# Performance work log

Measured on AMD Instinct MI355X. Metric: run time of the kernel, lower is better.

The kernel has to match this reference:

```python
import jax, jax.numpy as jnp
import numpy as np


def setup_inputs() -> dict:
    key = jax.random.key(0)
    ks = jax.random.split(key, 8)
    C, CK = 512, 64  # channels, att_channels = channels // 8
    B, H, W = 8, 64, 64
    x = jax.random.normal(ks[0], (B, C, H, W), dtype=jnp.float32)
    # 1x1 conv weights stored as [out, in] matrices
    s_in = 1.0 / np.sqrt(C)
    Wf_w = jax.random.uniform(ks[1], (CK, C), jnp.float32, -s_in, s_in)
    Wf_b = jax.random.uniform(ks[2], (CK,), jnp.float32, -s_in, s_in)
    Wg_w = jax.random.uniform(ks[3], (CK, C), jnp.float32, -s_in, s_in)
    Wg_b = jax.random.uniform(ks[4], (CK,), jnp.float32, -s_in, s_in)
    Wh_w = jax.random.uniform(ks[5], (C, C), jnp.float32, -s_in, s_in)
    Wh_b = jax.random.uniform(ks[6], (C,), jnp.float32, -s_in, s_in)
    gamma = jax.random.normal(ks[7], (1,), dtype=jnp.float32) * 0.1
    return {"x": x, "Wf_w": Wf_w, "Wf_b": Wf_b, "Wg_w": Wg_w, "Wg_b": Wg_b,
            "Wh_w": Wh_w, "Wh_b": Wh_b, "gamma": gamma}


def reference(x, Wf_w, Wf_b, Wg_w, Wg_b, Wh_w, Wh_b, gamma):
    B, C, H, W = x.shape
    N = H * W
    xt = x.reshape(B, C, N).transpose(0, 2, 1)           # [B, N, C]
    f = xt @ Wf_w.T + Wf_b                                # [B, N, Ck]
    g = xt @ Wg_w.T + Wg_b                                # [B, N, Ck]
    h = xt @ Wh_w.T + Wh_b                                # [B, N, C]
    scores = jnp.einsum('bnk,bmk->bnm', f, g)             # f @ g^T -> [B, N, N]
    beta = jax.nn.softmax(scores, axis=2)
    o = jnp.einsum('bnm,bmc->bnc', beta, h)               # [B, N, C]
    o = o.transpose(0, 2, 1).reshape(B, C, H, W)
    return gamma[0] * o + x
```

## Files before the change

kernel.cpp:

```cpp
#include <hip/hip_runtime.h>

typedef __attribute__((ext_vector_type(8))) short bf16x8;
typedef __attribute__((ext_vector_type(4))) float f32x4;
typedef __attribute__((ext_vector_type(16))) float f32x16;
typedef unsigned short u16;
typedef unsigned int u32;

namespace {
constexpr int kB = 8;
constexpr int kC = 512;
constexpr int kCK = 64;
constexpr int kN = 4096;

__device__ __forceinline__ u16 f2bf(float f) {
  union { float f; u32 u; } v; v.f = f;
  u32 r = v.u + 0x7fffu + ((v.u >> 16) & 1u);
  return (u16)(r >> 16);
}
__device__ __forceinline__ u32 pk2bf(float a, float b) {
  return (u32)f2bf(a) | ((u32)f2bf(b) << 16);
}
__device__ __forceinline__ f32x4 zero4() { f32x4 z = {0.f, 0.f, 0.f, 0.f}; return z; }
}

__global__ __launch_bounds__(256)
void wcast_kernel(const float* __restrict__ Wf, const float* __restrict__ Wg,
                  const float* __restrict__ Wh, u16* __restrict__ Wcat)
{
  const int idx = blockIdx.x * 256 + threadIdx.x;
  const int e = idx * 4;
  const int row = e >> 9, col = e & 511;
  const float* src = (row < 64) ? &Wf[(size_t)row * 512 + col]
                   : (row < 128) ? &Wg[(size_t)(row - 64) * 512 + col]
                                 : &Wh[(size_t)(row - 128) * 512 + col];
  const float4 v = *(const float4*)src;
  uint2 pk;
  pk.x = pk2bf(v.x, v.y);
  pk.y = pk2bf(v.z, v.w);
  *(uint2*)&Wcat[e] = pk;
}

__global__ __launch_bounds__(256, 2)
void fused_proj_kernel(const float* __restrict__ x, const u16* __restrict__ Wcat,
                       const float* __restrict__ Wf_b, const float* __restrict__ Wg_b,
                       const float* __restrict__ Wh_b,
                       u16* __restrict__ F, u16* __restrict__ G, u16* __restrict__ HT)
{
  const int t = threadIdx.x;
  const int nt = blockIdx.x, b = blockIdx.y;
  const int wave = t >> 6, lane = t & 63, lq = lane & 15, lk = lane >> 4;

  __shared__ __align__(16) u16 xt[64][536];

  const float* xb = x + (size_t)b * kC * kN + (size_t)nt * 64;
  for (int c0 = 0; c0 < kC; c0 += 16) {
    const int c = c0 + wave * 4;
    const size_t base = (size_t)c * kN + lane;
    const float v0 = xb[base];
    const float v1 = xb[base + kN];
    const float v2 = xb[base + 2 * (size_t)kN];
    const float v3 = xb[base + 3 * (size_t)kN];
    uint2 pk; pk.x = pk2bf(v0, v1); pk.y = pk2bf(v2, v3);
    *(uint2*)&xt[lane][c] = pk;
  }
  __syncthreads();

  f32x4 accF[4], accG[4], accH[8][4];
#pragma unroll
  for (int ni = 0; ni < 4; ++ni) { accF[ni] = zero4(); accG[ni] = zero4(); }
#pragma unroll
  for (int cj = 0; cj < 8; ++cj)
#pragma unroll
    for (int ni = 0; ni < 4; ++ni) accH[cj][ni] = zero4();

  for (int ks = 0; ks < 16; ++ks) {
    const int kb = ks * 32 + lk * 8;
    bf16x8 xf[4];
#pragma unroll
    for (int ni = 0; ni < 4; ++ni)
      xf[ni] = *(const bf16x8*)&xt[ni * 16 + lq][kb];

    const bf16x8 wf = *(const bf16x8*)&Wcat[(size_t)(wave * 16 + lq) * 512 + kb];
    const bf16x8 wg = *(const bf16x8*)&Wcat[(size_t)(64 + wave * 16 + lq) * 512 + kb];
    bf16x8 wh[8];
#pragma unroll
    for (int cj = 0; cj < 8; ++cj)
      wh[cj] = *(const bf16x8*)&Wcat[(size_t)(128 + wave * 128 + cj * 16 + lq) * 512 + kb];

#pragma unroll
    for (int ni = 0; ni < 4; ++ni) {
      accF[ni] = __builtin_amdgcn_mfma_f32_16x16x32_bf16(wf, xf[ni], accF[ni], 0, 0, 0);
      accG[ni] = __builtin_amdgcn_mfma_f32_16x16x32_bf16(wg, xf[ni], accG[ni], 0, 0, 0);
#pragma unroll
      for (int cj = 0; cj < 8; ++cj)
        accH[cj][ni] = __builtin_amdgcn_mfma_f32_16x16x32_bf16(xf[ni], wh[cj], accH[cj][ni], 0, 0, 0);
    }
  }

  u16* Fb = F + (size_t)b * kN * kCK;
  u16* Gb = G + (size_t)b * kN * kCK;
  u16* Hb = HT + (size_t)b * kC * kN;

  {
    const float4 bf = *(const float4*)&Wf_b[wave * 16 + lk * 4];
    const float4 bg = *(const float4*)&Wg_b[wave * 16 + lk * 4];
#pragma unroll
    for (int ni = 0; ni < 4; ++ni) {
      const size_t nrow = (size_t)(nt * 64 + ni * 16 + lq);
      uint2 pf, pg;
      pf.x = pk2bf(accF[ni][0] + bf.x, accF[ni][1] + bf.y);
      pf.y = pk2bf(accF[ni][2] + bf.z, accF[ni][3] + bf.w);
      pg.x = pk2bf(accG[ni][0] + bg.x, accG[ni][1] + bg.y);
      pg.y = pk2bf(accG[ni][2] + bg.z, accG[ni][3] + bg.w);
      *(uint2*)&Fb[nrow * kCK + wave * 16 + lk * 4] = pf;
      *(uint2*)&Gb[nrow * kCK + wave * 16 + lk * 4] = pg;
    }
  }
#pragma unroll
  for (int cj = 0; cj < 8; ++cj) {
    const int cout = wave * 128 + cj * 16 + lq;
    const float bh = Wh_b[cout];
#pragma unroll
    for (int ni = 0; ni < 4; ++ni) {
      uint2 ph;
      ph.x = pk2bf(accH[cj][ni][0] + bh, accH[cj][ni][1] + bh);
      ph.y = pk2bf(accH[cj][ni][2] + bh, accH[cj][ni][3] + bh);
      *(uint2*)&Hb[(size_t)cout * kN + nt * 64 + ni * 16 + lk * 4] = ph;
    }
  }
}

__global__ __launch_bounds__(512, 2)
void pv_kernel(const float* __restrict__ x, const u16* __restrict__ F,
               const u16* __restrict__ G, const u16* __restrict__ HT,
               const float* __restrict__ gamma, float* __restrict__ out)
{
  const int t = threadIdx.x;
  const int bid = blockIdx.x;
  const int b  = bid & 7;
  const int qt = bid >> 3;
  const int wave = t >> 6, lane = t & 63;
  const int lq = lane & 15, lk = lane >> 4;
  const int l31 = lane & 31, hi = lane >> 5;

  const int sq2 = wave & 3;
  const int sm2 = wave >> 2;

  const u16* Fb = F + (size_t)b * kN * kCK;
  const u16* Gb = G + (size_t)b * kN * kCK;
  const u16* Hb = HT + (size_t)b * kC * kN;

  __shared__ __align__(16) u16 Ps[2][128][72];
  __shared__ float Lred[2][128];

  const float g0 = gamma[0];

  bf16x8 fF[2][2];
#pragma unroll
  for (int ct = 0; ct < 2; ++ct)
#pragma unroll
    for (int kh = 0; kh < 2; ++kh)
      fF[ct][kh] = *(const bf16x8*)&Fb[(size_t)(qt * 128 + sq2 * 32 + ct * 16 + lq) * kCK + lk * 8 + kh * 32];

  f32x16 acc[2][4];
#pragma unroll
  for (int ci = 0; ci < 2; ++ci)
#pragma unroll
    for (int qb = 0; qb < 4; ++qb)
#pragma unroll
      for (int r = 0; r < 16; ++r) acc[ci][qb][r] = 0.f;

  float lsum[2] = {0.f, 0.f};

  bf16x8 gc[2][2];
#pragma unroll
  for (int ms = 0; ms < 2; ++ms)
#pragma unroll
    for (int kh = 0; kh < 2; ++kh)
      gc[ms][kh] = *(const bf16x8*)&Gb[(size_t)(sm2 * 32 + ms * 16 + lq) * kCK + lk * 8 + kh * 32];

  bf16x8 hc[2][4];

  {
    f32x4 s[2][2];
#pragma unroll
    for (int ms = 0; ms < 2; ++ms)
#pragma unroll
      for (int ct = 0; ct < 2; ++ct) {
        s[ms][ct] = zero4();
        s[ms][ct] = __builtin_amdgcn_mfma_f32_16x16x32_bf16(gc[ms][0], fF[ct][0], s[ms][ct], 0, 0, 0);
        s[ms][ct] = __builtin_amdgcn_mfma_f32_16x16x32_bf16(gc[ms][1], fF[ct][1], s[ms][ct], 0, 0, 0);
      }
#pragma unroll
    for (int ms = 0; ms < 2; ++ms)
#pragma unroll
      for (int kh = 0; kh < 2; ++kh)
        gc[ms][kh] = *(const bf16x8*)&Gb[(size_t)(64 + sm2 * 32 + ms * 16 + lq) * kCK + lk * 8 + kh * 32];
#pragma unroll
    for (int ms = 0; ms < 2; ++ms)
#pragma unroll
      for (int ct = 0; ct < 2; ++ct) {
        const float p0 = __expf(s[ms][ct][0]);
        const float p1 = __expf(s[ms][ct][1]);
        const float p2 = __expf(s[ms][ct][2]);
        const float p3 = __expf(s[ms][ct][3]);
        lsum[ct] += (p0 + p1) + (p2 + p3);
        uint2 pk; pk.x = pk2bf(p0, p1); pk.y = pk2bf(p2, p3);
        *(uint2*)&Ps[0][sq2 * 32 + ct * 16 + lq][sm2 * 32 + ms * 16 + lk * 4] = pk;
      }
#pragma unroll
    for (int ci = 0; ci < 2; ++ci) {
      const size_t hrow = (size_t)(wave * 64 + ci * 32 + l31) * kN;
#pragma unroll
      for (int ks = 0; ks < 4; ++ks)
        hc[ci][ks] = *(const bf16x8*)&Hb[hrow + ks * 16 + hi * 8];
    }
    asm volatile("s_waitcnt lgkmcnt(0)\n\ts_barrier" ::: "memory");
  }

  for (int mt = 1; mt < kN / 64; ++mt) {
    const int pb = (mt - 1) & 1;
    const int buf = mt & 1;

    f32x4 s[2][2];
#pragma unroll
    for (int ms = 0; ms < 2; ++ms)
#pragma unroll
      for (int ct = 0; ct < 2; ++ct) {
        s[ms][ct] = zero4();
        s[ms][ct] = __builtin_amdgcn_mfma_f32_16x16x32_bf16(gc[ms][0], fF[ct][0], s[ms][ct], 0, 0, 0);
        s[ms][ct] = __builtin_amdgcn_mfma_f32_16x16x32_bf16(gc[ms][1], fF[ct][1], s[ms][ct], 0, 0, 0);
      }

    {
      const int mtn = (mt + 1 < kN / 64) ? mt + 1 : mt;
#pragma unroll
      for (int ms = 0; ms < 2; ++ms)
#pragma unroll
        for (int kh = 0; kh < 2; ++kh)
          gc[ms][kh] = *(const bf16x8*)&Gb[(size_t)(mtn * 64 + sm2 * 32 + ms * 16 + lq) * kCK + lk * 8 + kh * 32];
    }

#pragma unroll
    for (int ks = 0; ks < 4; ++ks) {
      bf16x8 pB[4];
#pragma unroll
      for (int qb = 0; qb < 4; ++qb)
        pB[qb] = *(const bf16x8*)&Ps[pb][qb * 32 + l31][ks * 16 + hi * 8];
#pragma unroll
      for (int ci = 0; ci < 2; ++ci)
#pragma unroll
        for (int qb = 0; qb < 4; ++qb)
          acc[ci][qb] = __builtin_amdgcn_mfma_f32_32x32x16_bf16(hc[ci][ks], pB[qb], acc[ci][qb], 0, 0, 0);
      {
        const int ms = ks >> 1, ct = ks & 1;
        const float p0 = __expf(s[ms][ct][0]);
        const float p1 = __expf(s[ms][ct][1]);
        const float p2 = __expf(s[ms][ct][2]);
        const float p3 = __expf(s[ms][ct][3]);
        lsum[ct] += (p0 + p1) + (p2 + p3);
        uint2 pk; pk.x = pk2bf(p0, p1); pk.y = pk2bf(p2, p3);
        *(uint2*)&Ps[buf][sq2 * 32 + ct * 16 + lq][sm2 * 32 + ms * 16 + lk * 4] = pk;
      }
    }

#pragma unroll
    for (int ci = 0; ci < 2; ++ci) {
      const size_t hrow = (size_t)(wave * 64 + ci * 32 + l31) * kN + (size_t)mt * 64;
#pragma unroll
      for (int ks = 0; ks < 4; ++ks)
        hc[ci][ks] = *(const bf16x8*)&Hb[hrow + ks * 16 + hi * 8];
    }

    asm volatile("s_waitcnt lgkmcnt(0)\n\ts_barrier" ::: "memory");
  }

  {
    const int pb = (kN / 64 - 1) & 1;
#pragma unroll
    for (int ks = 0; ks < 4; ++ks) {
      bf16x8 pB[4];
#pragma unroll
      for (int qb = 0; qb < 4; ++qb)
        pB[qb] = *(const bf16x8*)&Ps[pb][qb * 32 + l31][ks * 16 + hi * 8];
#pragma unroll
      for (int ci = 0; ci < 2; ++ci)
#pragma unroll
        for (int qb = 0; qb < 4; ++qb)
          acc[ci][qb] = __builtin_amdgcn_mfma_f32_32x32x16_bf16(hc[ci][ks], pB[qb], acc[ci][qb], 0, 0, 0);
    }
  }

  float l0 = lsum[0], l1 = lsum[1];
  l0 += __shfl_xor(l0, 16); l0 += __shfl_xor(l0, 32);
  l1 += __shfl_xor(l1, 16); l1 += __shfl_xor(l1, 32);
  __syncthreads();
  if (lane < 16) {
    Lred[sm2][sq2 * 32 + lane] = l0;
    Lred[sm2][sq2 * 32 + 16 + lane] = l1;
  }
  __syncthreads();

  float rs[4];
#pragma unroll
  for (int qb = 0; qb < 4; ++qb)
    rs[qb] = 1.f / (Lred[0][qb * 32 + l31] + Lred[1][qb * 32 + l31]);

#pragma unroll
  for (int ci = 0; ci < 2; ++ci)
#pragma unroll
    for (int qb = 0; qb < 4; ++qb)
#pragma unroll
      for (int r = 0; r < 16; ++r) {
        const int crow = (r & 3) + 8 * (r >> 2) + 4 * hi;
        const int c = wave * 64 + ci * 32 + crow;
        const int n = qt * 128 + qb * 32 + l31;
        const size_t idx = ((size_t)b * kC + c) * kN + n;
        out[idx] = g0 * (acc[ci][qb][r] * rs[qb]) + x[idx];
      }
}

extern "C" void kernel_launch(void* const* d_in, const int* in_sizes, int n_in,
                              void* d_out, int out_size, void* d_ws, size_t ws_size,
                              hipStream_t stream)
{
  const float* x     = (const float*)d_in[0];
  const float* Wf_w  = (const float*)d_in[1];
  const float* Wf_b  = (const float*)d_in[2];
  const float* Wg_w  = (const float*)d_in[3];
  const float* Wg_b  = (const float*)d_in[4];
  const float* Wh_w  = (const float*)d_in[5];
  const float* Wh_b  = (const float*)d_in[6];
  const float* gamma = (const float*)d_in[7];
  float* out = (float*)d_out;

  const size_t nF = (size_t)kB * kN * kCK;
  const size_t nH = (size_t)kB * kC * kN;
  const size_t nW = 640 * 512;

  u16* F  = (u16*)d_ws;
  u16* G  = F + nF;
  u16* HT = G + nF;
  u16* Wcat = HT + nH;
  const size_t need = (2 * nF + nH + nW) * sizeof(u16);
  if (ws_size < need) return;

  wcast_kernel<<<dim3(nW / 1024), dim3(256), 0, stream>>>(Wf_w, Wg_w, Wh_w, Wcat);
  fused_proj_kernel<<<dim3(kN / 64, kB), dim3(256), 0, stream>>>(x, Wcat, Wf_b, Wg_b, Wh_b, F, G, HT);
  pv_kernel<<<dim3(256), dim3(512), 0, stream>>>(x, F, G, HT, gamma, out);
}
```

Baseline: 255.5 us.

## Double key tile to 128 and interleave H loads, exp and PV MFMAs

The key-tile width of the fused attention loop grows from 64 to 128, which halves the number of barrier-separated iterations. Score MFMAs are split into two halves per tile, and the H register loads are streamed per k-slice between PV MFMA groups, so global loads, exp/packing and matrix work interleave more finely. s_setprio is raised around the PV MFMA bursts. This enlarges the P shared buffer and adds register pressure, and the hand-ordered schedule may not map onto the hardware as intended.

```diff
diff --git a/kernel.cpp b/kernel.cpp
--- a/kernel.cpp
+++ b/kernel.cpp
@@ -11,6 +11,7 @@
 constexpr int kC = 512;
 constexpr int kCK = 64;
 constexpr int kN = 4096;
+constexpr int kNT = 32;
 
 __device__ __forceinline__ u16 f2bf(float f) {
   union { float f; u32 u; } v; v.f = f;
@@ -150,7 +151,7 @@
   const u16* Gb = G + (size_t)b * kN * kCK;
   const u16* Hb = HT + (size_t)b * kC * kN;
 
-  __shared__ __align__(16) u16 Ps[2][128][72];
+  __shared__ __align__(16) u16 Ps[2][128][136];
   __shared__ float Lred[2][128];
 
   const float g0 = gamma[0];
@@ -173,121 +174,132 @@
   float lsum[2] = {0.f, 0.f};
 
   bf16x8 gc[2][2];
-#pragma unroll
-  for (int ms = 0; ms < 2; ++ms)
-#pragma unroll
-    for (int kh = 0; kh < 2; ++kh)
-      gc[ms][kh] = *(const bf16x8*)&Gb[(size_t)(sm2 * 32 + ms * 16 + lq) * kCK + lk * 8 + kh * 32];
-
   bf16x8 hc[2][4];
+
+#define LOADG(pair, mtile)                                                        \
+  {                                                                               \
+    _Pragma("unroll")                                                             \
+    for (int ms = 0; ms < 2; ++ms)                                                \
+      _Pragma("unroll")                                                           \
+      for (int kh = 0; kh < 2; ++kh)                                              \
+        gc[ms][kh] = *(const bf16x8*)&Gb[(size_t)((mtile) * 128 + sm2 * 64 +      \
+            ((pair) * 2 + ms) * 16 + lq) * kCK + lk * 8 + kh * 32];               \
+  }
+#define LOADH(j, mtile, slice)                                                    \
+  {                                                                               \
+    _Pragma("unroll")                                                             \
+    for (int ci = 0; ci < 2; ++ci)                                                \
+      hc[ci][j] = *(const bf16x8*)&Hb[(size_t)(wave * 64 + ci * 32 + l31) * kN +  \
+          (size_t)(mtile) * 128 + (slice) * 16 + hi * 8];                         \
+  }
+#define SCOMP()                                                                   \
+  {                                                                               \
+    _Pragma("unroll")                                                             \
+    for (int ms = 0; ms < 2; ++ms)                                                \
+      _Pragma("unroll")                                                           \
+      for (int ct = 0; ct < 2; ++ct) {                                            \
+        s[ms][ct] = zero4();                                                      \
+        s[ms][ct] = __builtin_amdgcn_mfma_f32_16x16x32_bf16(gc[ms][0], fF[ct][0], s[ms][ct], 0, 0, 0); \
+        s[ms][ct] = __builtin_amdgcn_mfma_f32_16x16x32_bf16(gc[ms][1], fF[ct][1], s[ms][ct], 0, 0, 0); \
+      }                                                                           \
+  }
+#define EXPW(sv, ct, msG, buf)                                                    \
+  {                                                                               \
+    const float p0 = __expf((sv)[0]);                                             \
+    const float p1 = __expf((sv)[1]);                                             \
+    const float p2 = __expf((sv)[2]);                                             \
+    const float p3 = __expf((sv)[3]);                                             \
+    lsum[ct] += (p0 + p1) + (p2 + p3);                                            \
+    uint2 pk; pk.x = pk2bf(p0, p1); pk.y = pk2bf(p2, p3);                         \
+    *(uint2*)&Ps[buf][sq2 * 32 + (ct) * 16 + lq][sm2 * 64 + (msG) * 16 + lk * 4] = pk; \
+  }
+#define PV8(h0, h1, pB)                                                           \
+  {                                                                               \
+    __builtin_amdgcn_s_setprio(1);                                                \
+    _Pragma("unroll")                                                             \
+    for (int qb = 0; qb < 4; ++qb)                                                \
+      acc[0][qb] = __builtin_amdgcn_mfma_f32_32x32x16_bf16(h0, pB[qb], acc[0][qb], 0, 0, 0); \
+    _Pragma("unroll")                                                             \
+    for (int qb = 0; qb < 4; ++qb)                                                \
+      acc[1][qb] = __builtin_amdgcn_mfma_f32_32x32x16_bf16(h1, pB[qb], acc[1][qb], 0, 0, 0); \
+    __builtin_amdgcn_s_setprio(0);                                                \
+  }
+#define RDPB(pB, Pr, col)                                                         \
+  {                                                                               \
+    _Pragma("unroll")                                                             \
+    for (int qb = 0; qb < 4; ++qb)                                                \
+      pB[qb] = *(const bf16x8*)&Pr[qb * 32 + l31][col];                           \
+  }
 
   {
     f32x4 s[2][2];
-#pragma unroll
-    for (int ms = 0; ms < 2; ++ms)
-#pragma unroll
-      for (int ct = 0; ct < 2; ++ct) {
-        s[ms][ct] = zero4();
-        s[ms][ct] = __builtin_amdgcn_mfma_f32_16x16x32_bf16(gc[ms][0], fF[ct][0], s[ms][ct], 0, 0, 0);
-        s[ms][ct] = __builtin_amdgcn_mfma_f32_16x16x32_bf16(gc[ms][1], fF[ct][1], s[ms][ct], 0, 0, 0);
-      }
-#pragma unroll
-    for (int ms = 0; ms < 2; ++ms)
-#pragma unroll
-      for (int kh = 0; kh < 2; ++kh)
-        gc[ms][kh] = *(const bf16x8*)&Gb[(size_t)(64 + sm2 * 32 + ms * 16 + lq) * kCK + lk * 8 + kh * 32];
-#pragma unroll
-    for (int ms = 0; ms < 2; ++ms)
-#pragma unroll
-      for (int ct = 0; ct < 2; ++ct) {
-        const float p0 = __expf(s[ms][ct][0]);
-        const float p1 = __expf(s[ms][ct][1]);
-        const float p2 = __expf(s[ms][ct][2]);
-        const float p3 = __expf(s[ms][ct][3]);
-        lsum[ct] += (p0 + p1) + (p2 + p3);
-        uint2 pk; pk.x = pk2bf(p0, p1); pk.y = pk2bf(p2, p3);
-        *(uint2*)&Ps[0][sq2 * 32 + ct * 16 + lq][sm2 * 32 + ms * 16 + lk * 4] = pk;
-      }
-#pragma unroll
-    for (int ci = 0; ci < 2; ++ci) {
-      const size_t hrow = (size_t)(wave * 64 + ci * 32 + l31) * kN;
-#pragma unroll
-      for (int ks = 0; ks < 4; ++ks)
-        hc[ci][ks] = *(const bf16x8*)&Hb[hrow + ks * 16 + hi * 8];
-    }
+    LOADG(0, 0);
+    SCOMP();
+    LOADG(1, 0);
+#pragma unroll
+    for (int ks = 0; ks < 4; ++ks)
+      EXPW(s[ks >> 1][ks & 1], (ks & 1), (ks >> 1), 0);
+    SCOMP();
+    LOADG(0, 1);
+#pragma unroll
+    for (int ks = 4; ks < 8; ++ks)
+      EXPW(s[(ks - 4) >> 1][ks & 1], (ks & 1), (ks >> 1), 0);
+#pragma unroll
+    for (int j = 0; j < 4; ++j)
+      LOADH(j, 0, j);
     asm volatile("s_waitcnt lgkmcnt(0)\n\ts_barrier" ::: "memory");
   }
 
-  for (int mt = 1; mt < kN / 64; ++mt) {
+  for (int mt = 1; mt < kNT; ++mt) {
     const int pb = (mt - 1) & 1;
     const int buf = mt & 1;
+    const u16 (*Pr)[136] = Ps[pb];
 
     f32x4 s[2][2];
-#pragma unroll
-    for (int ms = 0; ms < 2; ++ms)
-#pragma unroll
-      for (int ct = 0; ct < 2; ++ct) {
-        s[ms][ct] = zero4();
-        s[ms][ct] = __builtin_amdgcn_mfma_f32_16x16x32_bf16(gc[ms][0], fF[ct][0], s[ms][ct], 0, 0, 0);
-        s[ms][ct] = __builtin_amdgcn_mfma_f32_16x16x32_bf16(gc[ms][1], fF[ct][1], s[ms][ct], 0, 0, 0);
-      }
-
-    {
-      const int mtn = (mt + 1 < kN / 64) ? mt + 1 : mt;
-#pragma unroll
-      for (int ms = 0; ms < 2; ++ms)
-#pragma unroll
-        for (int kh = 0; kh < 2; ++kh)
-          gc[ms][kh] = *(const bf16x8*)&Gb[(size_t)(mtn * 64 + sm2 * 32 + ms * 16 + lq) * kCK + lk * 8 + kh * 32];
-    }
+    SCOMP();
+    LOADG(1, mt);
 
 #pragma unroll
     for (int ks = 0; ks < 4; ++ks) {
       bf16x8 pB[4];
-#pragma unroll
-      for (int qb = 0; qb < 4; ++qb)
-        pB[qb] = *(const bf16x8*)&Ps[pb][qb * 32 + l31][ks * 16 + hi * 8];
-#pragma unroll
-      for (int ci = 0; ci < 2; ++ci)
-#pragma unroll
-        for (int qb = 0; qb < 4; ++qb)
-          acc[ci][qb] = __builtin_amdgcn_mfma_f32_32x32x16_bf16(hc[ci][ks], pB[qb], acc[ci][qb], 0, 0, 0);
-      {
-        const int ms = ks >> 1, ct = ks & 1;
-        const float p0 = __expf(s[ms][ct][0]);
-        const float p1 = __expf(s[ms][ct][1]);
-        const float p2 = __expf(s[ms][ct][2]);
-        const float p3 = __expf(s[ms][ct][3]);
-        lsum[ct] += (p0 + p1) + (p2 + p3);
-        uint2 pk; pk.x = pk2bf(p0, p1); pk.y = pk2bf(p2, p3);
-        *(uint2*)&Ps[buf][sq2 * 32 + ct * 16 + lq][sm2 * 32 + ms * 16 + lk * 4] = pk;
-      }
-    }
-
-#pragma unroll
-    for (int ci = 0; ci < 2; ++ci) {
-      const size_t hrow = (size_t)(wave * 64 + ci * 32 + l31) * kN + (size_t)mt * 64;
-#pragma unroll
-      for (int ks = 0; ks < 4; ++ks)
-        hc[ci][ks] = *(const bf16x8*)&Hb[hrow + ks * 16 + hi * 8];
+      RDPB(pB, Pr, ks * 16 + hi * 8);
+      EXPW(s[ks >> 1][ks & 1], (ks & 1), (ks >> 1), buf);
+      PV8(hc[0][ks], hc[1][ks], pB);
+      LOADH(ks, mt - 1, ks + 4);
+    }
+
+    SCOMP();
+    {
+      const int mtn = (mt + 1 < kNT) ? mt + 1 : mt;
+      LOADG(0, mtn);
+    }
+
+#pragma unroll
+    for (int ks = 4; ks < 8; ++ks) {
+      bf16x8 pB[4];
+      RDPB(pB, Pr, ks * 16 + hi * 8);
+      EXPW(s[(ks - 4) >> 1][ks & 1], (ks & 1), (ks >> 1), buf);
+      PV8(hc[0][ks & 3], hc[1][ks & 3], pB);
+      LOADH((ks & 3), mt, ks - 4);
     }
 
     asm volatile("s_waitcnt lgkmcnt(0)\n\ts_barrier" ::: "memory");
   }
 
   {
-    const int pb = (kN / 64 - 1) & 1;
+    const u16 (*Pr)[136] = Ps[(kNT - 1) & 1];
 #pragma unroll
     for (int ks = 0; ks < 4; ++ks) {
       bf16x8 pB[4];
-#pragma unroll
-      for (int qb = 0; qb < 4; ++qb)
-        pB[qb] = *(const bf16x8*)&Ps[pb][qb * 32 + l31][ks * 16 + hi * 8];
-#pragma unroll
-      for (int ci = 0; ci < 2; ++ci)
-#pragma unroll
-        for (int qb = 0; qb < 4; ++qb)
-          acc[ci][qb] = __builtin_amdgcn_mfma_f32_32x32x16_bf16(hc[ci][ks], pB[qb], acc[ci][qb], 0, 0, 0);
+      RDPB(pB, Pr, ks * 16 + hi * 8);
+      PV8(hc[0][ks], hc[1][ks], pB);
+      LOADH(ks, kNT - 1, ks + 4);
+    }
+#pragma unroll
+    for (int ks = 4; ks < 8; ++ks) {
+      bf16x8 pB[4];
+      RDPB(pB, Pr, ks * 16 + hi * 8);
+      PV8(hc[0][ks & 3], hc[1][ks & 3], pB);
     }
   }
 
@@ -318,6 +330,12 @@
         const size_t idx = ((size_t)b * kC + c) * kN + n;
         out[idx] = g0 * (acc[ci][qb][r] * rs[qb]) + x[idx];
       }
+#undef LOADG
+#undef LOADH
+#undef SCOMP
+#undef EXPW
+#undef PV8
+#undef RDPB
 }
 
 extern "C" void kernel_launch(void* const* d_in, const int* in_sizes, int n_in,
```

After: 319.0 us. +24.8%, slower.
